# Kernel tuning notes

Hardware: AMD Instinct MI355X
Metric: run time of the kernel (lower is better)

Reference implementation:

```python
import jax, jax.numpy as jnp
import numpy as np

T, B, DIN, DH, DOUT = 512, 256, 128, 512, 128


def setup_inputs() -> dict:
    key = jax.random.key(0)
    k1, k2, k3, k4 = jax.random.split(key, 4)
    xs = jax.random.normal(k1, (T, B, DIN), dtype=jnp.float32)
    W1x = 0.1 * jax.random.normal(k2, (DIN, DH), dtype=jnp.float32)
    # random orthogonal init for the recurrent weight, as in the original
    q, _ = jnp.linalg.qr(jax.random.normal(k3, (DH, DH), dtype=jnp.float32))
    W1h = q.astype(jnp.float32)
    b1 = jnp.zeros([], dtype=jnp.float32)
    W2 = 0.1 * jax.random.normal(k4, (DH, DOUT), dtype=jnp.float32)
    b2 = jnp.zeros([], dtype=jnp.float32)
    return {"xs": xs, "W1x": W1x, "W1h": W1h, "b1": b1, "W2": W2, "b2": b2}


def reference(xs, W1x, W1h, b1, W2, b2):
    # Precompute all input projections in one big GEMM: [T, B, DH]
    xproj = jnp.einsum('tbi,ih->tbh', xs, W1x)
    h0 = jnp.zeros((xs.shape[1], W1h.shape[0]), dtype=xs.dtype)

    def step(h, xp):
        h_new = jnp.tanh(xp + h @ W1h + b1)
        return h_new, None

    h_final, _ = jax.lax.scan(step, h0, xproj)
    return h_final @ W2 + b2
```

## Files before the change

### kernel.cpp

```cpp
#include <hip/hip_runtime.h>

#define T_STEPS 512
#define BATCH   256
#define DIN     128
#define DH      512
#define DOUT    128
#define RGRP    16

typedef __attribute__((ext_vector_type(8))) short  short8;
typedef __attribute__((ext_vector_type(4))) float  floatx4;

union Pack8 { short8 s; unsigned short h[8]; };

__device__ __forceinline__ float bf2f(unsigned short u) {
    union { unsigned int i; float f; } v; v.i = ((unsigned int)u) << 16; return v.f;
}
__device__ __forceinline__ unsigned short f2bf(float f) {
    union { float f; unsigned int i; } v; v.f = f;
    unsigned int b = v.i;
    b += 0x7FFFu + ((b >> 16) & 1u);
    return (unsigned short)(b >> 16);
}
__device__ __forceinline__ float fast_tanh(float v) {
    float ex = __expf(v + v);
    return 1.f - 2.f / (ex + 1.f);
}

__global__ void pack_b_kernel(const float* __restrict__ W,
                              unsigned short* __restrict__ Wp, int K, int N) {
    int idx = blockIdx.x * blockDim.x + threadIdx.x;
    if (idx >= K * N) return;
    int k = idx / N, n = idx % N;
    int nt = n >> 4, kc = k >> 5, quad = (k >> 3) & 3, j = k & 7;
    int lane = quad * 16 + (n & 15);
    int KC = K >> 5;
    Wp[((size_t)(nt * KC + kc) * 64 + lane) * 8 + j] = f2bf(W[idx]);
}

__global__ __launch_bounds__(256) void xproj_kernel(
        const float* __restrict__ xs,
        const unsigned short* __restrict__ W1xp,
        unsigned short* __restrict__ xp) {
    const int tid  = threadIdx.x;
    const int lane = tid & 63;
    const int w    = tid >> 6;
    const int m    = lane & 15;
    const int q    = lane >> 4;
    const long row0 = (long)blockIdx.x * 16;

    short8 a[4];
#pragma unroll
    for (int kc = 0; kc < 4; ++kc) {
        const float* src = xs + (row0 + m) * DIN + kc * 32 + q * 8;
        Pack8 av;
#pragma unroll
        for (int j = 0; j < 8; ++j) av.h[j] = f2bf(src[j]);
        a[kc] = av.s;
    }

#pragma unroll
    for (int i = 0; i < 8; ++i) {
        const int nt = w * 8 + i;
        floatx4 acc = {0.f, 0.f, 0.f, 0.f};
#pragma unroll
        for (int kc = 0; kc < 4; ++kc) {
            short8 b = *(const short8*)(W1xp + ((size_t)(nt * 4 + kc) * 64 + lane) * 8);
            acc = __builtin_amdgcn_mfma_f32_16x16x32_bf16(a[kc], b, acc, 0, 0, 0);
        }
#pragma unroll
        for (int r = 0; r < 4; ++r)
            xp[(row0 + q * 4 + r) * DH + nt * 16 + m] = f2bf(acc[r]);
    }
}

template <int LKC>
__global__ __launch_bounds__(512, 2) void rnn_kernel(
        const unsigned short* __restrict__ xp,
        const unsigned short* __restrict__ W1hp,
        const float* __restrict__ b1p,
        const float* __restrict__ W2,
        const float* __restrict__ b2p,
        float* __restrict__ out) {
    extern __shared__ unsigned short smem[];
    unsigned short* Hb = smem;
    unsigned short* Wl = smem + 2 * 16 * 520;
#define HB(b, r, c) Hb[(b) * 8320 + (r) * 520 + (c)]

    const int tid  = threadIdx.x;
    const int lane = tid & 63;
    const int w    = tid >> 6;
    const int m    = lane & 15;
    const int q    = lane >> 4;
    const int rg   = blockIdx.x;
    const float b1 = b1p[0];

    short8 bfr[8][4];
#pragma unroll
    for (int kc = 0; kc < 8; ++kc)
#pragma unroll
        for (int i = 0; i < 4; ++i)
            bfr[kc][i] = *(const short8*)(W1hp +
                ((size_t)((4 * w + i) * 16 + kc) * 64 + lane) * 8);

    if (LKC > 0) {
        for (int c = tid; c < LKC * 2048; c += 512) {
            int j = c >> 11;
            int r = c & 2047;
            int nt = r >> 6, ln = r & 63;
            *(short8*)&Wl[(size_t)c * 8] =
                *(const short8*)(W1hp + ((size_t)(nt * 16 + 8 + j) * 64 + ln) * 8);
        }
    }

    for (int c = tid; c < 1024; c += 512) {
        int row = c >> 6, cc = c & 63;
        const unsigned short* src = xp + (size_t)(rg * 16 + row) * DH + cc * 8;
        Pack8 pk;
#pragma unroll
        for (int j = 0; j < 8; ++j) pk.h[j] = f2bf(fast_tanh(bf2f(src[j]) + b1));
        *(short8*)&HB(0, row, cc * 8) = pk.s;
    }
    __syncthreads();

    constexpr int KB = 8 + LKC;
    constexpr int NG = (8 - LKC + 1) / 2;

    int p = 0;
#pragma unroll 1
    for (int t = 1; t < T_STEPS; ++t) {
        short8 sb[2][2][4];
#pragma unroll
        for (int g = 0; g < 2 && g < NG; ++g)
#pragma unroll
            for (int c = 0; c < 2; ++c) {
                int kc = KB + 2 * g + c;
                if (kc < 16)
#pragma unroll
                    for (int i = 0; i < 4; ++i)
                        sb[g][c][i] = *(const short8*)(W1hp +
                            ((size_t)((4 * w + i) * 16 + kc) * 64 + lane) * 8);
            }

        unsigned short xv[4][4];
#pragma unroll
        for (int i = 0; i < 4; ++i)
#pragma unroll
            for (int r = 0; r < 4; ++r)
                xv[i][r] = xp[((size_t)t * BATCH + rg * 16 + q * 4 + r) * DH +
                              (4 * w + i) * 16 + m];

        floatx4 acc[4];
#pragma unroll
        for (int i = 0; i < 4; ++i) acc[i] = (floatx4){0.f, 0.f, 0.f, 0.f};

#pragma unroll
        for (int kc = 0; kc < 8; ++kc) {
            short8 a = *(const short8*)&HB(p, m, kc * 32 + q * 8);
#pragma unroll
            for (int i = 0; i < 4; ++i)
                acc[i] = __builtin_amdgcn_mfma_f32_16x16x32_bf16(a, bfr[kc][i], acc[i], 0, 0, 0);
        }

#pragma unroll
        for (int j = 0; j < LKC; ++j) {
            short8 a = *(const short8*)&HB(p, m, (8 + j) * 32 + q * 8);
#pragma unroll
            for (int i = 0; i < 4; ++i) {
                short8 b = *(const short8*)&Wl[((size_t)(j * 32 + 4 * w + i) * 64 + lane) * 8];
                acc[i] = __builtin_amdgcn_mfma_f32_16x16x32_bf16(a, b, acc[i], 0, 0, 0);
            }
        }

#pragma unroll
        for (int g = 0; g < NG; ++g) {
#pragma unroll
            for (int c = 0; c < 2; ++c) {
                int kc = KB + 2 * g + c;
                if (kc < 16) {
                    short8 a = *(const short8*)&HB(p, m, kc * 32 + q * 8);
#pragma unroll
                    for (int i = 0; i < 4; ++i)
                        acc[i] = __builtin_amdgcn_mfma_f32_16x16x32_bf16(a, sb[g & 1][c][i], acc[i], 0, 0, 0);
                }
            }
            if (g + 2 < NG) {
#pragma unroll
                for (int c = 0; c < 2; ++c) {
                    int kc = KB + 2 * (g + 2) + c;
                    if (kc < 16)
#pragma unroll
                        for (int i = 0; i < 4; ++i)
                            sb[g & 1][c][i] = *(const short8*)(W1hp +
                                ((size_t)((4 * w + i) * 16 + kc) * 64 + lane) * 8);
                }
            }
        }

#pragma unroll
        for (int i = 0; i < 4; ++i)
#pragma unroll
            for (int r = 0; r < 4; ++r) {
                float v = acc[i][r] + bf2f(xv[i][r]) + b1;
                HB(1 - p, q * 4 + r, (4 * w + i) * 16 + m) = f2bf(fast_tanh(v));
            }
        __syncthreads();
        p ^= 1;
    }

    const float b2 = b2p[0];
    floatx4 acc = {0.f, 0.f, 0.f, 0.f};
#pragma unroll
    for (int kc = 0; kc < 16; ++kc) {
        short8 av = *(const short8*)&HB(p, m, kc * 32 + q * 8);
        Pack8 bv;
#pragma unroll
        for (int j = 0; j < 8; ++j)
            bv.h[j] = f2bf(W2[(size_t)(kc * 32 + q * 8 + j) * DOUT + w * 16 + m]);
        acc = __builtin_amdgcn_mfma_f32_16x16x32_bf16(av, bv.s, acc, 0, 0, 0);
    }
#pragma unroll
    for (int r = 0; r < 4; ++r)
        out[(size_t)(rg * 16 + q * 4 + r) * DOUT + w * 16 + m] = acc[r] + b2;
#undef HB
}

extern "C" void kernel_launch(void* const* d_in, const int* in_sizes, int n_in,
                              void* d_out, int out_size, void* d_ws, size_t ws_size,
                              hipStream_t stream) {
    const float* xs  = (const float*)d_in[0];
    const float* W1x = (const float*)d_in[1];
    const float* W1h = (const float*)d_in[2];
    const float* b1  = (const float*)d_in[3];
    const float* W2  = (const float*)d_in[4];
    const float* b2  = (const float*)d_in[5];
    float* out = (float*)d_out;

    unsigned short* xp   = (unsigned short*)d_ws;
    unsigned short* w1hp = xp + (size_t)T_STEPS * BATCH * DH;
    unsigned short* w1xp = w1hp + (size_t)DH * DH;

    pack_b_kernel<<<(DH * DH + 255) / 256, 256, 0, stream>>>(W1h, w1hp, DH, DH);
    pack_b_kernel<<<(DIN * DH + 255) / 256, 256, 0, stream>>>(W1x, w1xp, DIN, DH);
    xproj_kernel<<<(T_STEPS * BATCH) / 16, 256, 0, stream>>>(xs, w1xp, xp);

    constexpr size_t SMEM_BIG   = 2 * 16 * 520 * 2 + 3 * 32 * 64 * 8 * 2;
    constexpr size_t SMEM_SMALL = 2 * 16 * 520 * 2;
    hipError_t e = hipFuncSetAttribute(
        reinterpret_cast<const void*>(&rnn_kernel<3>),
        hipFuncAttributeMaxDynamicSharedMemorySize, (int)SMEM_BIG);
    if (e == hipSuccess) {
        rnn_kernel<3><<<RGRP, 512, SMEM_BIG, stream>>>(xp, w1hp, b1, W2, b2, out);
    } else {
        rnn_kernel<0><<<RGRP, 512, SMEM_SMALL, stream>>>(xp, w1hp, b1, W2, b2, out);
    }
}
```

Baseline: 1.684 ms.

## Halve RNN block to 4 waves with 8 N-tiles each and fragment-ordered xproj

The recurrent kernel now runs 256 threads per block, each wave owning 8 output tiles. More W1h k-chunks stay register-resident (10 instead of 8), plus 3 in LDS and the rest streamed from global. The xproj output is stored in MFMA-fragment order so each lane reads one 64-bit word per tile instead of scattered 16-bit loads. W2 is prepacked to bf16 for the final GEMM, the bf16 rounding is simplified to round-half-up, and the LDS row padding changes. The aim is less per-step global load and sync overhead, at the cost of higher register pressure and fewer waves to hide latency.

```diff
diff --git a/kernel.cpp b/kernel.cpp
--- a/kernel.cpp
+++ b/kernel.cpp
@@ -11,15 +11,14 @@
 typedef __attribute__((ext_vector_type(4))) float  floatx4;
 
 union Pack8 { short8 s; unsigned short h[8]; };
+union Pack4 { unsigned long long u; unsigned short h[4]; };
 
 __device__ __forceinline__ float bf2f(unsigned short u) {
     union { unsigned int i; float f; } v; v.i = ((unsigned int)u) << 16; return v.f;
 }
 __device__ __forceinline__ unsigned short f2bf(float f) {
     union { float f; unsigned int i; } v; v.f = f;
-    unsigned int b = v.i;
-    b += 0x7FFFu + ((b >> 16) & 1u);
-    return (unsigned short)(b >> 16);
+    return (unsigned short)((v.i + 0x8000u) >> 16);
 }
 __device__ __forceinline__ float fast_tanh(float v) {
     float ex = __expf(v + v);
@@ -37,10 +36,14 @@
     Wp[((size_t)(nt * KC + kc) * 64 + lane) * 8 + j] = f2bf(W[idx]);
 }
 
+__device__ __forceinline__ size_t xpidx(int tb_blk, int w, int i, int lane) {
+    return (((size_t)tb_blk * 4 + w) * 8 + i) * 64 + lane;
+}
+
 __global__ __launch_bounds__(256) void xproj_kernel(
         const float* __restrict__ xs,
         const unsigned short* __restrict__ W1xp,
-        unsigned short* __restrict__ xp) {
+        unsigned long long* __restrict__ xq) {
     const int tid  = threadIdx.x;
     const int lane = tid & 63;
     const int w    = tid >> 6;
@@ -67,24 +70,26 @@
             short8 b = *(const short8*)(W1xp + ((size_t)(nt * 4 + kc) * 64 + lane) * 8);
             acc = __builtin_amdgcn_mfma_f32_16x16x32_bf16(a[kc], b, acc, 0, 0, 0);
         }
-#pragma unroll
-        for (int r = 0; r < 4; ++r)
-            xp[(row0 + q * 4 + r) * DH + nt * 16 + m] = f2bf(acc[r]);
+        Pack4 pk;
+#pragma unroll
+        for (int r = 0; r < 4; ++r) pk.h[r] = f2bf(acc[r]);
+        xq[xpidx(blockIdx.x, w, i, lane)] = pk.u;
     }
 }
 
 template <int LKC>
-__global__ __launch_bounds__(512, 2) void rnn_kernel(
-        const unsigned short* __restrict__ xp,
+__global__ __launch_bounds__(256, 1) void rnn_kernel(
+        const unsigned long long* __restrict__ xq,
         const unsigned short* __restrict__ W1hp,
         const float* __restrict__ b1p,
-        const float* __restrict__ W2,
+        const unsigned short* __restrict__ W2p,
         const float* __restrict__ b2p,
         float* __restrict__ out) {
     extern __shared__ unsigned short smem[];
     unsigned short* Hb = smem;
-    unsigned short* Wl = smem + 2 * 16 * 520;
-#define HB(b, r, c) Hb[(b) * 8320 + (r) * 520 + (c)]
+    unsigned short* Wl = smem + 2 * 16 * 516;
+#define HROW 516
+#define HBUF 8256
 
     const int tid  = threadIdx.x;
     const int lane = tid & 63;
@@ -93,135 +98,119 @@
     const int q    = lane >> 4;
     const int rg   = blockIdx.x;
     const float b1 = b1p[0];
-
-    short8 bfr[8][4];
-#pragma unroll
-    for (int kc = 0; kc < 8; ++kc)
-#pragma unroll
-        for (int i = 0; i < 4; ++i)
+    constexpr int RKC  = 10;
+    constexpr int SKC0 = RKC + LKC;
+
+    short8 bfr[RKC][8];
+#pragma unroll
+    for (int kc = 0; kc < RKC; ++kc)
+#pragma unroll
+        for (int i = 0; i < 8; ++i)
             bfr[kc][i] = *(const short8*)(W1hp +
-                ((size_t)((4 * w + i) * 16 + kc) * 64 + lane) * 8);
+                ((size_t)((8 * w + i) * 16 + kc) * 64 + lane) * 8);
 
     if (LKC > 0) {
-        for (int c = tid; c < LKC * 2048; c += 512) {
-            int j = c >> 11;
-            int r = c & 2047;
+        for (int c = tid; c < LKC * 2048; c += 256) {
+            int j = c >> 11, r = c & 2047;
             int nt = r >> 6, ln = r & 63;
             *(short8*)&Wl[(size_t)c * 8] =
-                *(const short8*)(W1hp + ((size_t)(nt * 16 + 8 + j) * 64 + ln) * 8);
-        }
-    }
-
-    for (int c = tid; c < 1024; c += 512) {
-        int row = c >> 6, cc = c & 63;
-        const unsigned short* src = xp + (size_t)(rg * 16 + row) * DH + cc * 8;
-        Pack8 pk;
-#pragma unroll
-        for (int j = 0; j < 8; ++j) pk.h[j] = f2bf(fast_tanh(bf2f(src[j]) + b1));
-        *(short8*)&HB(0, row, cc * 8) = pk.s;
+                *(const short8*)(W1hp + ((size_t)(nt * 16 + RKC + j) * 64 + ln) * 8);
+        }
+    }
+
+#pragma unroll
+    for (int i = 0; i < 8; ++i) {
+        Pack4 xv; xv.u = xq[xpidx(0 * 16 + rg, w, i, lane)];
+#pragma unroll
+        for (int r = 0; r < 4; ++r)
+            Hb[(q * 4 + r) * HROW + (8 * w + i) * 16 + m] =
+                f2bf(fast_tanh(bf2f(xv.h[r]) + b1));
     }
     __syncthreads();
-
-    constexpr int KB = 8 + LKC;
-    constexpr int NG = (8 - LKC + 1) / 2;
 
     int p = 0;
 #pragma unroll 1
     for (int t = 1; t < T_STEPS; ++t) {
-        short8 sb[2][2][4];
-#pragma unroll
-        for (int g = 0; g < 2 && g < NG; ++g)
-#pragma unroll
-            for (int c = 0; c < 2; ++c) {
-                int kc = KB + 2 * g + c;
-                if (kc < 16)
-#pragma unroll
-                    for (int i = 0; i < 4; ++i)
-                        sb[g][c][i] = *(const short8*)(W1hp +
-                            ((size_t)((4 * w + i) * 16 + kc) * 64 + lane) * 8);
-            }
-
-        unsigned short xv[4][4];
-#pragma unroll
-        for (int i = 0; i < 4; ++i)
-#pragma unroll
-            for (int r = 0; r < 4; ++r)
-                xv[i][r] = xp[((size_t)t * BATCH + rg * 16 + q * 4 + r) * DH +
-                              (4 * w + i) * 16 + m];
-
-        floatx4 acc[4];
-#pragma unroll
-        for (int i = 0; i < 4; ++i) acc[i] = (floatx4){0.f, 0.f, 0.f, 0.f};
-
-#pragma unroll
-        for (int kc = 0; kc < 8; ++kc) {
-            short8 a = *(const short8*)&HB(p, m, kc * 32 + q * 8);
-#pragma unroll
-            for (int i = 0; i < 4; ++i)
+        Pack4 xv[8];
+#pragma unroll
+        for (int i = 0; i < 8; ++i)
+            xv[i].u = xq[xpidx(t * 16 + rg, w, i, lane)];
+
+        short8 sb[8];
+        if (SKC0 < 16) {
+#pragma unroll
+            for (int i = 0; i < 8; ++i)
+                sb[i] = *(const short8*)(W1hp +
+                    ((size_t)((8 * w + i) * 16 + SKC0) * 64 + lane) * 8);
+        }
+
+        floatx4 acc[8];
+#pragma unroll
+        for (int i = 0; i < 8; ++i) acc[i] = (floatx4){0.f, 0.f, 0.f, 0.f};
+
+#pragma unroll
+        for (int kc = 0; kc < RKC; ++kc) {
+            short8 a = *(const short8*)&Hb[p * HBUF + m * HROW + kc * 32 + q * 8];
+#pragma unroll
+            for (int i = 0; i < 8; ++i)
                 acc[i] = __builtin_amdgcn_mfma_f32_16x16x32_bf16(a, bfr[kc][i], acc[i], 0, 0, 0);
         }
-
 #pragma unroll
         for (int j = 0; j < LKC; ++j) {
-            short8 a = *(const short8*)&HB(p, m, (8 + j) * 32 + q * 8);
-#pragma unroll
-            for (int i = 0; i < 4; ++i) {
-                short8 b = *(const short8*)&Wl[((size_t)(j * 32 + 4 * w + i) * 64 + lane) * 8];
+            short8 a = *(const short8*)&Hb[p * HBUF + m * HROW + (RKC + j) * 32 + q * 8];
+#pragma unroll
+            for (int i = 0; i < 8; ++i) {
+                short8 b = *(const short8*)&Wl[((size_t)(j * 32 + 8 * w + i) * 64 + lane) * 8];
                 acc[i] = __builtin_amdgcn_mfma_f32_16x16x32_bf16(a, b, acc[i], 0, 0, 0);
             }
         }
-
-#pragma unroll
-        for (int g = 0; g < NG; ++g) {
-#pragma unroll
-            for (int c = 0; c < 2; ++c) {
-                int kc = KB + 2 * g + c;
-                if (kc < 16) {
-                    short8 a = *(const short8*)&HB(p, m, kc * 32 + q * 8);
-#pragma unroll
-                    for (int i = 0; i < 4; ++i)
-                        acc[i] = __builtin_amdgcn_mfma_f32_16x16x32_bf16(a, sb[g & 1][c][i], acc[i], 0, 0, 0);
-                }
+#pragma unroll
+        for (int s = SKC0; s < 16; ++s) {
+            short8 a = *(const short8*)&Hb[p * HBUF + m * HROW + s * 32 + q * 8];
+#pragma unroll
+            for (int i = 0; i < 8; ++i)
+                acc[i] = __builtin_amdgcn_mfma_f32_16x16x32_bf16(a, sb[i], acc[i], 0, 0, 0);
+            if (s + 1 < 16) {
+#pragma unroll
+                for (int i = 0; i < 8; ++i)
+                    sb[i] = *(const short8*)(W1hp +
+                        ((size_t)((8 * w + i) * 16 + s + 1) * 64 + lane) * 8);
             }
-            if (g + 2 < NG) {
-#pragma unroll
-                for (int c = 0; c < 2; ++c) {
-                    int kc = KB + 2 * (g + 2) + c;
-                    if (kc < 16)
-#pragma unroll
-                        for (int i = 0; i < 4; ++i)
-                            sb[g & 1][c][i] = *(const short8*)(W1hp +
-                                ((size_t)((4 * w + i) * 16 + kc) * 64 + lane) * 8);
-                }
-            }
-        }
-
-#pragma unroll
-        for (int i = 0; i < 4; ++i)
+        }
+
+        unsigned short* hd = &Hb[(1 - p) * HBUF];
+#pragma unroll
+        for (int i = 0; i < 8; ++i)
 #pragma unroll
             for (int r = 0; r < 4; ++r) {
-                float v = acc[i][r] + bf2f(xv[i][r]) + b1;
-                HB(1 - p, q * 4 + r, (4 * w + i) * 16 + m) = f2bf(fast_tanh(v));
+                float v = acc[i][r] + bf2f(xv[i].h[r]) + b1;
+                hd[(q * 4 + r) * HROW + (8 * w + i) * 16 + m] = f2bf(fast_tanh(v));
             }
         __syncthreads();
         p ^= 1;
     }
 
     const float b2 = b2p[0];
-    floatx4 acc = {0.f, 0.f, 0.f, 0.f};
+    floatx4 ao[2];
+#pragma unroll
+    for (int u = 0; u < 2; ++u) ao[u] = (floatx4){0.f, 0.f, 0.f, 0.f};
 #pragma unroll
     for (int kc = 0; kc < 16; ++kc) {
-        short8 av = *(const short8*)&HB(p, m, kc * 32 + q * 8);
-        Pack8 bv;
-#pragma unroll
-        for (int j = 0; j < 8; ++j)
-            bv.h[j] = f2bf(W2[(size_t)(kc * 32 + q * 8 + j) * DOUT + w * 16 + m]);
-        acc = __builtin_amdgcn_mfma_f32_16x16x32_bf16(av, bv.s, acc, 0, 0, 0);
-    }
-#pragma unroll
-    for (int r = 0; r < 4; ++r)
-        out[(size_t)(rg * 16 + q * 4 + r) * DOUT + w * 16 + m] = acc[r] + b2;
-#undef HB
+        short8 a = *(const short8*)&Hb[p * HBUF + m * HROW + kc * 32 + q * 8];
+#pragma unroll
+        for (int u = 0; u < 2; ++u) {
+            short8 b = *(const short8*)(W2p +
+                ((size_t)((2 * w + u) * 16 + kc) * 64 + lane) * 8);
+            ao[u] = __builtin_amdgcn_mfma_f32_16x16x32_bf16(a, b, ao[u], 0, 0, 0);
+        }
+    }
+#pragma unroll
+    for (int u = 0; u < 2; ++u)
+#pragma unroll
+        for (int r = 0; r < 4; ++r)
+            out[(size_t)(rg * 16 + q * 4 + r) * DOUT + (2 * w + u) * 16 + m] = ao[u][r] + b2;
+#undef HROW
+#undef HBUF
 }
 
 extern "C" void kernel_launch(void* const* d_in, const int* in_sizes, int n_in,
@@ -235,22 +224,27 @@
     const float* b2  = (const float*)d_in[5];
     float* out = (float*)d_out;
 
-    unsigned short* xp   = (unsigned short*)d_ws;
-    unsigned short* w1hp = xp + (size_t)T_STEPS * BATCH * DH;
+    unsigned short* xp2  = (unsigned short*)d_ws;
+    unsigned short* w1hp = xp2 + (size_t)T_STEPS * BATCH * DH;
     unsigned short* w1xp = w1hp + (size_t)DH * DH;
+    unsigned short* w2p  = w1xp + (size_t)DIN * DH;
 
     pack_b_kernel<<<(DH * DH + 255) / 256, 256, 0, stream>>>(W1h, w1hp, DH, DH);
     pack_b_kernel<<<(DIN * DH + 255) / 256, 256, 0, stream>>>(W1x, w1xp, DIN, DH);
-    xproj_kernel<<<(T_STEPS * BATCH) / 16, 256, 0, stream>>>(xs, w1xp, xp);
-
-    constexpr size_t SMEM_BIG   = 2 * 16 * 520 * 2 + 3 * 32 * 64 * 8 * 2;
-    constexpr size_t SMEM_SMALL = 2 * 16 * 520 * 2;
+    pack_b_kernel<<<(DH * DOUT + 255) / 256, 256, 0, stream>>>(W2, w2p, DH, DOUT);
+    xproj_kernel<<<(T_STEPS * BATCH) / 16, 256, 0, stream>>>(
+        xs, w1xp, (unsigned long long*)xp2);
+
+    constexpr size_t SMEM_BIG   = (2 * 16 * 516 + 3 * 2048 * 8) * 2;
+    constexpr size_t SMEM_SMALL = 2 * 16 * 516 * 2;
     hipError_t e = hipFuncSetAttribute(
         reinterpret_cast<const void*>(&rnn_kernel<3>),
         hipFuncAttributeMaxDynamicSharedMemorySize, (int)SMEM_BIG);
     if (e == hipSuccess) {
-        rnn_kernel<3><<<RGRP, 512, SMEM_BIG, stream>>>(xp, w1hp, b1, W2, b2, out);
+        rnn_kernel<3><<<RGRP, 256, SMEM_BIG, stream>>>(
+            (const unsigned long long*)xp2, w1hp, b1, w2p, b2, out);
     } else {
-        rnn_kernel<0><<<RGRP, 512, SMEM_SMALL, stream>>>(xp, w1hp, b1, W2, b2, out);
-    }
-}
+        rnn_kernel<0><<<RGRP, 256, SMEM_SMALL, stream>>>(
+            (const unsigned long long*)xp2, w1hp, b1, w2p, b2, out);
+    }
+}
```

After: 2.291 ms. +36.0%, slower.
